# Performance work log

Hardware: AMD Instinct MI355X
Metric: run time of the kernel (lower is better)

## Reference

```python
import jax, jax.numpy as jnp
import numpy as np

# Instant-NGP HashGrid constants (match tcnn encoding_config defaults in the module)
N_LEVELS = 16
N_FEATS = 2
LOG2_T = 16
T = 1 << LOG2_T            # hashmap entries per level
BASE_RES = 16
PER_LEVEL_SCALE = 1.5
N_POINTS = 1 << 20
PRIMES = (1, 2654435761, 805459861)  # tcnn spatial-hash primes

# 8 corner offsets of the unit cube, [8,3]
_CORNERS = np.array([[i, j, k] for i in (0, 1) for j in (0, 1) for k in (0, 1)], dtype=np.float32)


def setup_inputs() -> dict:
    key = jax.random.key(0)
    k1, k2 = jax.random.split(key)
    x = jax.random.uniform(k1, (N_POINTS, 3), dtype=jnp.float32)
    # tcnn initializes hash tables uniform in [-1e-4, 1e-4]
    table = jax.random.uniform(k2, (N_LEVELS, T, N_FEATS), minval=-1e-4, maxval=1e-4, dtype=jnp.float32)
    return {"x": x, "table": table}


def _corner_index(grid, res, dense):
    # grid: [N,8,3] int32 corner coordinates -> [N,8] table index
    if dense:
        g = jnp.clip(grid, 0, res - 1)
        return g[..., 0] + g[..., 1] * res + g[..., 2] * res * res
    g = grid.astype(jnp.uint32)
    h = (g[..., 0] * jnp.uint32(PRIMES[0])
         ^ g[..., 1] * jnp.uint32(PRIMES[1])
         ^ g[..., 2] * jnp.uint32(PRIMES[2]))
    return (h & jnp.uint32(T - 1)).astype(jnp.int32)


def _hashgrid_forward(x, table):
    x = x.astype(jnp.float32)
    offs = jnp.asarray(_CORNERS)                      # [8,3]
    outs = []
    for level in range(N_LEVELS):
        # tcnn: grid_scale = base * s^level - 1 ; resolution = ceil(scale)+1
        scale = float(BASE_RES * (PER_LEVEL_SCALE ** level) - 1.0)
        res = int(np.ceil(scale)) + 1
        dense = res ** 3 <= T                          # tcnn uses dense indexing when the grid fits
        pos = x * scale + 0.5                          # [N,3]
        g0 = jnp.floor(pos)
        frac = pos - g0                                # [N,3] trilinear fractions
        grid = (g0[:, None, :] + offs[None]).astype(jnp.int32)   # [N,8,3]
        idx = _corner_index(grid, res, dense)          # [N,8]
        feat = table[level][idx]                       # [N,8,F] irregular gather
        # trilinear weights: prod over dims of frac or (1-frac) per corner
        w = jnp.prod(jnp.where(offs[None] > 0, frac[:, None, :], 1.0 - frac[:, None, :]), axis=-1)  # [N,8]
        outs.append(jnp.sum(w[..., None] * feat, axis=1))        # [N,F]
    return jnp.concatenate(outs, axis=-1)              # [N, L*F] = [N,32]


def reference(x, table):
    return _hashgrid_forward(x, table)
```

## Files before the change

### kernel.cpp

```cpp
#include <hip/hip_runtime.h>
#include <stdint.h>


#define NLVL 16
#define TS 65536
#define P2 2654435761u
#define P3 805459861u

__constant__ float C_SCALES[NLVL] = {
    15.0f, 23.0f, 35.0f, 53.0f, 80.0f, 120.5f, 181.25f, 272.375f,
    409.0625f, 614.09375f, 921.640625f, 1382.9609375f,
    2074.94140625f, 3112.912109375f, 4669.8681640625f, 7005.30224609375f};

__device__ __forceinline__ float2 f4lo(float4 v) { return make_float2(v.x, v.y); }
__device__ __forceinline__ float2 f4hi(float4 v) { return make_float2(v.z, v.w); }

__device__ __forceinline__ void lds_put2(float* s_out, int p, int f2,
                                         float a, float b) {
    const int sw = p & 31;
    const int base = p * 32 + (f2 ^ (sw & 30));
    if (sw & 1) { s_out[base] = b; s_out[base + 1] = a; }
    else        { s_out[base] = a; s_out[base + 1] = b; }
}

__global__ __launch_bounds__(256, 5) void hashgrid_fwd(
    const float* __restrict__ x,
    const float* __restrict__ table,
    float* __restrict__ out,
    int n)
{
    __shared__ float s_out[256 * 32];

    const int tid0 = blockIdx.x * 256 + threadIdx.x;
    const int tid = min(tid0, n - 1);
    const int p = threadIdx.x;

    const float px = x[3 * tid + 0];
    const float py = x[3 * tid + 1];
    const float pz = x[3 * tid + 2];

    {
        const int RESO[3] = {16, 24, 36};
        const float DSC[3] = {15.0f, 23.0f, 35.0f};
#pragma unroll
        for (int l = 0; l < 3; ++l) {
            const float scale = DSC[l];
            const float fx = px * scale + 0.5f;
            const float fy = py * scale + 0.5f;
            const float fz = pz * scale + 0.5f;
            const float gx = floorf(fx), gy = floorf(fy), gz = floorf(fz);
            const float wx = fx - gx, wy = fy - gy, wz = fz - gz;
            const int ix = (int)gx, iy = (int)gy, iz = (int)gz;

            const float2* tbl = ((const float2*)table) + (size_t)l * TS;
            const int R = RESO[l];
            const int x0 = min(ix, R - 1);
            const int y0 = min(iy, R - 1), y1 = min(iy + 1, R - 1);
            const int z0 = min(iz, R - 1), z1 = min(iz + 1, R - 1);
            const int xb = min(x0, R - 2);
            const bool hi0 = (x0 != xb);
            const int y0R = y0 * R, y1R = y1 * R;
            const int z0R = z0 * R * R, z1R = z1 * R * R;
            const float4 f00 = *(const float4*)(tbl + (xb + y0R + z0R));
            const float4 f01 = *(const float4*)(tbl + (xb + y0R + z1R));
            const float4 f10 = *(const float4*)(tbl + (xb + y1R + z0R));
            const float4 f11 = *(const float4*)(tbl + (xb + y1R + z1R));
            const float2 c0 = hi0 ? f4hi(f00) : f4lo(f00), c4 = f4hi(f00);
            const float2 c1 = hi0 ? f4hi(f01) : f4lo(f01), c5 = f4hi(f01);
            const float2 c2 = hi0 ? f4hi(f10) : f4lo(f10), c6 = f4hi(f10);
            const float2 c3 = hi0 ? f4hi(f11) : f4lo(f11), c7 = f4hi(f11);

            const float ux = 1.0f - wx, uy = 1.0f - wy, uz = 1.0f - wz;
            const float w0 = ux * uy * uz, w1 = ux * uy * wz;
            const float w2 = ux * wy * uz, w3 = ux * wy * wz;
            const float w4 = wx * uy * uz, w5 = wx * uy * wz;
            const float w6 = wx * wy * uz, w7 = wx * wy * wz;

            const float o0 = w0 * c0.x + w1 * c1.x + w2 * c2.x + w3 * c3.x +
                             w4 * c4.x + w5 * c5.x + w6 * c6.x + w7 * c7.x;
            const float o1 = w0 * c0.y + w1 * c1.y + w2 * c2.y + w3 * c3.y +
                             w4 * c4.y + w5 * c5.y + w6 * c6.y + w7 * c7.y;
            lds_put2(s_out, p, 2 * l, o0, o1);
        }
    }

#pragma unroll 2
    for (int l = 3; l < NLVL; ++l) {
        const float scale = C_SCALES[l];
        const float fx = px * scale + 0.5f;
        const float fy = py * scale + 0.5f;
        const float fz = pz * scale + 0.5f;
        const float gx = floorf(fx), gy = floorf(fy), gz = floorf(fz);
        const float wx = fx - gx, wy = fy - gy, wz = fz - gz;
        const int ix = (int)gx, iy = (int)gy, iz = (int)gz;

        const float2* tbl = ((const float2*)table) + (size_t)l * TS;

        const uint32_t bx = (uint32_t)ix;
        const uint32_t hy0 = (uint32_t)iy * P2, hy1 = hy0 + P2;
        const uint32_t hz0 = (uint32_t)iz * P3, hz1 = hz0 + P3;
        const uint32_t b00 = hy0 ^ hz0, b01 = hy0 ^ hz1;
        const uint32_t b10 = hy1 ^ hz0, b11 = hy1 ^ hz1;
        const uint32_t i00 = (bx ^ b00) & (TS - 1);
        const uint32_t i01 = (bx ^ b01) & (TS - 1);
        const uint32_t i10 = (bx ^ b10) & (TS - 1);
        const uint32_t i11 = (bx ^ b11) & (TS - 1);
        const float4* tbl4 = (const float4*)tbl;
        const float4 f00 = tbl4[i00 >> 1];
        const float4 f01 = tbl4[i01 >> 1];
        const float4 f10 = tbl4[i10 >> 1];
        const float4 f11 = tbl4[i11 >> 1];
        const float2 c0 = (i00 & 1) ? f4hi(f00) : f4lo(f00);
        const float2 c1 = (i01 & 1) ? f4hi(f01) : f4lo(f01);
        const float2 c2 = (i10 & 1) ? f4hi(f10) : f4lo(f10);
        const float2 c3 = (i11 & 1) ? f4hi(f11) : f4lo(f11);
        float2 c4, c5, c6, c7;
        if ((ix & 1) == 0) {
            c4 = (i00 & 1) ? f4lo(f00) : f4hi(f00);
            c5 = (i01 & 1) ? f4lo(f01) : f4hi(f01);
            c6 = (i10 & 1) ? f4lo(f10) : f4hi(f10);
            c7 = (i11 & 1) ? f4lo(f11) : f4hi(f11);
        } else {
            const uint32_t bx1 = bx + 1;
            c4 = tbl[(bx1 ^ b00) & (TS - 1)];
            c5 = tbl[(bx1 ^ b01) & (TS - 1)];
            c6 = tbl[(bx1 ^ b10) & (TS - 1)];
            c7 = tbl[(bx1 ^ b11) & (TS - 1)];
        }

        const float ux = 1.0f - wx, uy = 1.0f - wy, uz = 1.0f - wz;
        const float w0 = ux * uy * uz, w1 = ux * uy * wz;
        const float w2 = ux * wy * uz, w3 = ux * wy * wz;
        const float w4 = wx * uy * uz, w5 = wx * uy * wz;
        const float w6 = wx * wy * uz, w7 = wx * wy * wz;

        const float o0 = w0 * c0.x + w1 * c1.x + w2 * c2.x + w3 * c3.x +
                         w4 * c4.x + w5 * c5.x + w6 * c6.x + w7 * c7.x;
        const float o1 = w0 * c0.y + w1 * c1.y + w2 * c2.y + w3 * c3.y +
                         w4 * c4.y + w5 * c5.y + w6 * c6.y + w7 * c7.y;
        lds_put2(s_out, p, 2 * l, o0, o1);
    }

    __syncthreads();

    float* outb = out + (size_t)blockIdx.x * (256 * 32);
    const long long lim = (long long)n * 32 - (long long)blockIdx.x * (256 * 32);
#pragma unroll
    for (int r = 0; r < 32; ++r) {
        const int g = r * 256 + threadIdx.x;
        const int pp = g >> 5, f = g & 31;
        const float v = s_out[pp * 32 + (f ^ (pp & 31))];
        if (g < lim) outb[g] = v;
    }
}

extern "C" void kernel_launch(void* const* d_in, const int* in_sizes, int n_in,
                              void* d_out, int out_size, void* d_ws, size_t ws_size,
                              hipStream_t stream) {
    const float* x = (const float*)d_in[0];
    const float* table = (const float*)d_in[1];
    float* out = (float*)d_out;
    const int n = in_sizes[0] / 3;
    const int block = 256;
    const int grid = (n + block - 1) / block;
    hashgrid_fwd<<<grid, block, 0, stream>>>(x, table, out, n);
}
```

Before: 528.2 us.

## Use 128-thread blocks, nontemporal table loads, and vectorized float4 output stores

Block size drops from 256 to 128 threads and the shared-memory staging layout is redone with an 8-slot rotation, so the output write-back uses 16-byte vector stores instead of scalar ones. The hashed-level table gathers become nontemporal loads, which hint the cache to not retain them. The aim is fewer store instructions, less LDS per block for higher occupancy, and less cache pollution. Nontemporal loads on a 16 MB table that gets reused across points may reduce cache hit rates. There is also an odd leftover variable c3 that is computed but discarded.

```diff
diff --git a/kernel.cpp b/kernel.cpp
--- a/kernel.cpp
+++ b/kernel.cpp
@@ -7,31 +7,34 @@
 #define P2 2654435761u
 #define P3 805459861u
 
+typedef float v4f __attribute__((ext_vector_type(4)));
+typedef float v2f __attribute__((ext_vector_type(2)));
+
 __constant__ float C_SCALES[NLVL] = {
     15.0f, 23.0f, 35.0f, 53.0f, 80.0f, 120.5f, 181.25f, 272.375f,
     409.0625f, 614.09375f, 921.640625f, 1382.9609375f,
     2074.94140625f, 3112.912109375f, 4669.8681640625f, 7005.30224609375f};
 
-__device__ __forceinline__ float2 f4lo(float4 v) { return make_float2(v.x, v.y); }
-__device__ __forceinline__ float2 f4hi(float4 v) { return make_float2(v.z, v.w); }
+__device__ __forceinline__ v2f v4lo(v4f v) { v2f r; r.x = v.x; r.y = v.y; return r; }
+__device__ __forceinline__ v2f v4hi(v4f v) { v2f r; r.x = v.z; r.y = v.w; return r; }
 
-__device__ __forceinline__ void lds_put2(float* s_out, int p, int f2,
+__device__ __forceinline__ void lds_put2(float* s_out, int p, int l,
                                          float a, float b) {
-    const int sw = p & 31;
-    const int base = p * 32 + (f2 ^ (sw & 30));
-    if (sw & 1) { s_out[base] = b; s_out[base + 1] = a; }
-    else        { s_out[base] = a; s_out[base + 1] = b; }
+    const int slot = ((l >> 1) + p) & 7;
+    const int a32 = p * 32 + slot * 4 + (l & 1) * 2;
+    s_out[a32] = a;
+    s_out[a32 + 1] = b;
 }
 
-__global__ __launch_bounds__(256, 5) void hashgrid_fwd(
+__global__ __launch_bounds__(128, 5) void hashgrid_fwd(
     const float* __restrict__ x,
     const float* __restrict__ table,
     float* __restrict__ out,
     int n)
 {
-    __shared__ float s_out[256 * 32];
+    __shared__ float s_out[128 * 32];
 
-    const int tid0 = blockIdx.x * 256 + threadIdx.x;
+    const int tid0 = blockIdx.x * 128 + threadIdx.x;
     const int tid = min(tid0, n - 1);
     const int p = threadIdx.x;
 
@@ -52,7 +55,7 @@
             const float wx = fx - gx, wy = fy - gy, wz = fz - gz;
             const int ix = (int)gx, iy = (int)gy, iz = (int)gz;
 
-            const float2* tbl = ((const float2*)table) + (size_t)l * TS;
+            const v2f* tbl = ((const v2f*)table) + (size_t)l * TS;
             const int R = RESO[l];
             const int x0 = min(ix, R - 1);
             const int y0 = min(iy, R - 1), y1 = min(iy + 1, R - 1);
@@ -61,14 +64,14 @@
             const bool hi0 = (x0 != xb);
             const int y0R = y0 * R, y1R = y1 * R;
             const int z0R = z0 * R * R, z1R = z1 * R * R;
-            const float4 f00 = *(const float4*)(tbl + (xb + y0R + z0R));
-            const float4 f01 = *(const float4*)(tbl + (xb + y0R + z1R));
-            const float4 f10 = *(const float4*)(tbl + (xb + y1R + z0R));
-            const float4 f11 = *(const float4*)(tbl + (xb + y1R + z1R));
-            const float2 c0 = hi0 ? f4hi(f00) : f4lo(f00), c4 = f4hi(f00);
-            const float2 c1 = hi0 ? f4hi(f01) : f4lo(f01), c5 = f4hi(f01);
-            const float2 c2 = hi0 ? f4hi(f10) : f4lo(f10), c6 = f4hi(f10);
-            const float2 c3 = hi0 ? f4hi(f11) : f4lo(f11), c7 = f4hi(f11);
+            const v4f f00 = *(const v4f*)(tbl + (xb + y0R + z0R));
+            const v4f f01 = *(const v4f*)(tbl + (xb + y0R + z1R));
+            const v4f f10 = *(const v4f*)(tbl + (xb + y1R + z0R));
+            const v4f f11 = *(const v4f*)(tbl + (xb + y1R + z1R));
+            const v2f c0 = hi0 ? v4hi(f00) : v4lo(f00), c4 = v4hi(f00);
+            const v2f c1 = hi0 ? v4hi(f01) : v4lo(f01), c5 = v4hi(f01);
+            const v2f c2 = hi0 ? v4hi(f10) : v4lo(f10), c6 = v4hi(f10);
+            const v2f c3 = hi0 ? v4hi(f11) : v4lo(f11), c7 = v4hi(f11);
 
             const float ux = 1.0f - wx, uy = 1.0f - wy, uz = 1.0f - wz;
             const float w0 = ux * uy * uz, w1 = ux * uy * wz;
@@ -80,7 +83,7 @@
                              w4 * c4.x + w5 * c5.x + w6 * c6.x + w7 * c7.x;
             const float o1 = w0 * c0.y + w1 * c1.y + w2 * c2.y + w3 * c3.y +
                              w4 * c4.y + w5 * c5.y + w6 * c6.y + w7 * c7.y;
-            lds_put2(s_out, p, 2 * l, o0, o1);
+            lds_put2(s_out, p, l, o0, o1);
         }
     }
 
@@ -94,7 +97,7 @@
         const float wx = fx - gx, wy = fy - gy, wz = fz - gz;
         const int ix = (int)gx, iy = (int)gy, iz = (int)gz;
 
-        const float2* tbl = ((const float2*)table) + (size_t)l * TS;
+        const v2f* tbl = ((const v2f*)table) + (size_t)l * TS;
 
         const uint32_t bx = (uint32_t)ix;
         const uint32_t hy0 = (uint32_t)iy * P2, hy1 = hy0 + P2;
@@ -105,27 +108,28 @@
         const uint32_t i01 = (bx ^ b01) & (TS - 1);
         const uint32_t i10 = (bx ^ b10) & (TS - 1);
         const uint32_t i11 = (bx ^ b11) & (TS - 1);
-        const float4* tbl4 = (const float4*)tbl;
-        const float4 f00 = tbl4[i00 >> 1];
-        const float4 f01 = tbl4[i01 >> 1];
-        const float4 f10 = tbl4[i10 >> 1];
-        const float4 f11 = tbl4[i11 >> 1];
-        const float2 c0 = (i00 & 1) ? f4hi(f00) : f4lo(f00);
-        const float2 c1 = (i01 & 1) ? f4hi(f01) : f4lo(f01);
-        const float2 c2 = (i10 & 1) ? f4hi(f10) : f4lo(f10);
-        const float2 c3 = (i11 & 1) ? f4hi(f11) : f4lo(f11);
-        float2 c4, c5, c6, c7;
+        const v4f* tbl4 = (const v4f*)tbl;
+        const v4f f00 = __builtin_nontemporal_load(tbl4 + (i00 >> 1));
+        const v4f f01 = __builtin_nontemporal_load(tbl4 + (i01 >> 1));
+        const v4f f10 = __builtin_nontemporal_load(tbl4 + (i10 >> 1));
+        const v4f f11 = __builtin_nontemporal_load(tbl4 + (i11 >> 1));
+        const v2f c0 = (i00 & 1) ? v4hi(f00) : v4lo(f00);
+        const v2f c1 = (i01 & 1) ? v4hi(f01) : v4lo(f01);
+        const v2f c2 = (i10 & 1) ? v4hi(f10) : v4lo(f10);
+        const v2f c3 = (i11 & 1) ? v4hi(f10) : v4lo(f10);
+        v2f c3x = (i11 & 1) ? v4hi(f11) : v4lo(f11);
+        v2f c4, c5, c6, c7;
         if ((ix & 1) == 0) {
-            c4 = (i00 & 1) ? f4lo(f00) : f4hi(f00);
-            c5 = (i01 & 1) ? f4lo(f01) : f4hi(f01);
-            c6 = (i10 & 1) ? f4lo(f10) : f4hi(f10);
-            c7 = (i11 & 1) ? f4lo(f11) : f4hi(f11);
+            c4 = (i00 & 1) ? v4lo(f00) : v4hi(f00);
+            c5 = (i01 & 1) ? v4lo(f01) : v4hi(f01);
+            c6 = (i10 & 1) ? v4lo(f10) : v4hi(f10);
+            c7 = (i11 & 1) ? v4lo(f11) : v4hi(f11);
         } else {
             const uint32_t bx1 = bx + 1;
-            c4 = tbl[(bx1 ^ b00) & (TS - 1)];
-            c5 = tbl[(bx1 ^ b01) & (TS - 1)];
-            c6 = tbl[(bx1 ^ b10) & (TS - 1)];
-            c7 = tbl[(bx1 ^ b11) & (TS - 1)];
+            c4 = __builtin_nontemporal_load(tbl + ((bx1 ^ b00) & (TS - 1)));
+            c5 = __builtin_nontemporal_load(tbl + ((bx1 ^ b01) & (TS - 1)));
+            c6 = __builtin_nontemporal_load(tbl + ((bx1 ^ b10) & (TS - 1)));
+            c7 = __builtin_nontemporal_load(tbl + ((bx1 ^ b11) & (TS - 1)));
         }
 
         const float ux = 1.0f - wx, uy = 1.0f - wy, uz = 1.0f - wz;
@@ -134,23 +138,26 @@
         const float w4 = wx * uy * uz, w5 = wx * uy * wz;
         const float w6 = wx * wy * uz, w7 = wx * wy * wz;
 
-        const float o0 = w0 * c0.x + w1 * c1.x + w2 * c2.x + w3 * c3.x +
+        const float o0 = w0 * c0.x + w1 * c1.x + w2 * c2.x + w3 * c3x.x +
                          w4 * c4.x + w5 * c5.x + w6 * c6.x + w7 * c7.x;
-        const float o1 = w0 * c0.y + w1 * c1.y + w2 * c2.y + w3 * c3.y +
+        const float o1 = w0 * c0.y + w1 * c1.y + w2 * c2.y + w3 * c3x.y +
                          w4 * c4.y + w5 * c5.y + w6 * c6.y + w7 * c7.y;
-        lds_put2(s_out, p, 2 * l, o0, o1);
+        (void)c3;
+        lds_put2(s_out, p, l, o0, o1);
     }
 
     __syncthreads();
 
-    float* outb = out + (size_t)blockIdx.x * (256 * 32);
-    const long long lim = (long long)n * 32 - (long long)blockIdx.x * (256 * 32);
+    v4f* outb4 = (v4f*)(out + (size_t)blockIdx.x * (128 * 32));
+    const long long lim4 =
+        ((long long)n * 8) - (long long)blockIdx.x * (128 * 8);
 #pragma unroll
-    for (int r = 0; r < 32; ++r) {
-        const int g = r * 256 + threadIdx.x;
-        const int pp = g >> 5, f = g & 31;
-        const float v = s_out[pp * 32 + (f ^ (pp & 31))];
-        if (g < lim) outb[g] = v;
+    for (int r = 0; r < 8; ++r) {
+        const int e = r * 128 + threadIdx.x;
+        const int pp = e >> 3, g = e & 7;
+        const int slot = (g + pp) & 7;
+        const v4f v = *(const v4f*)&s_out[pp * 32 + slot * 4];
+        if (e < lim4) outb4[e] = v;
     }
 }
 
@@ -161,7 +168,7 @@
     const float* table = (const float*)d_in[1];
     float* out = (float*)d_out;
     const int n = in_sizes[0] / 3;
-    const int block = 256;
+    const int block = 128;
     const int grid = (n + block - 1) / block;
     hashgrid_fwd<<<grid, block, 0, stream>>>(x, table, out, n);
 }
```

Measured after the change: 1.235 ms. 134% more time.
